# Kernel optimization log

Hardware: AMD Instinct MI355X
Metric: run time of the kernel (lower is better)

## Reference

```python
import jax, jax.numpy as jnp
import numpy as np

B, T, D = 64, 512, 256   # batch, time, input feat
H = 256                  # LSTM hidden (features)


def setup_inputs() -> dict:
    key = jax.random.key(0)
    ks = jax.random.split(key, 16)
    s = lambda k, shp, fan: jax.random.normal(k, shp, jnp.float32) / np.sqrt(fan)
    return {
        "x":  jax.random.normal(ks[0], (B, T, D), jnp.float32),
        # LSTM params: fused gates order (i, f, g, o)
        "Wi": s(ks[1], (D, 4 * H), D),
        "Wh": s(ks[2], (H, 4 * H), H),
        "b":  jnp.zeros((4 * H,), jnp.float32),
        # single-head attention (head_dim = H)
        "Wq": s(ks[3], (H, H), H), "bq": jnp.zeros((H,), jnp.float32),
        "Wk": s(ks[4], (H, H), H), "bk": jnp.zeros((H,), jnp.float32),
        "Wv": s(ks[5], (H, H), H), "bv": jnp.zeros((H,), jnp.float32),
        "Wo": s(ks[6], (H, H), H), "bo": jnp.zeros((H,), jnp.float32),
        # MLP head
        "W1": s(ks[7], (H, 32), H), "b1": jnp.zeros((32,), jnp.float32),
        "W2": s(ks[8], (32, 3), 32), "b2": jnp.zeros((3,), jnp.float32),
    }


def _lstm_scan(x, Wi, Wh, b):
    # Precompute input-to-hidden projection for all timesteps (batched GEMM)
    xg = jnp.einsum('btd,dg->btg', x, Wi) + b          # [B,T,4H]
    c0 = jnp.zeros((x.shape[0], Wh.shape[0]), x.dtype)
    h0 = jnp.zeros_like(c0)

    def step(carry, xg_t):
        c, h = carry
        g = xg_t + h @ Wh                               # [B,4H]
        i, f, gg, o = jnp.split(g, 4, axis=-1)          # flax gate order i,f,g,o
        c = jax.nn.sigmoid(f) * c + jax.nn.sigmoid(i) * jnp.tanh(gg)
        h = jax.nn.sigmoid(o) * jnp.tanh(c)
        return (c, h), h

    (_, _), hs = jax.lax.scan(step, (c0, h0), jnp.swapaxes(xg, 0, 1))
    return jnp.swapaxes(hs, 0, 1)                       # [B,T,H]


def reference(x, Wi, Wh, b, Wq, bq, Wk, bk, Wv, bv, Wo, bo, W1, b1, W2, b2):
    h = _lstm_scan(x, Wi, Wh, b)                        # [B,T,H]
    # single-head dot-product attention (self-attention)
    q = h @ Wq + bq
    k = h @ Wk + bk
    v = h @ Wv + bv
    scale = 1.0 / np.sqrt(q.shape[-1]).astype(np.float32)
    scores = jnp.einsum('bqd,bkd->bqk', q * scale, k)   # [B,T,T]
    attn = jax.nn.softmax(scores, axis=-1)
    o = jnp.einsum('bqk,bkd->bqd', attn, v)
    o = o @ Wo + bo                                     # output projection
    # head on first timestep
    z = jax.nn.relu(o[:, 0, :] @ W1 + b1)
    return z @ W2 + b2                                  # [B,3]
```

## Files before the change

### kernel.cpp

```cpp
#include <hip/hip_runtime.h>
#include <hip/hip_bf16.h>


typedef __attribute__((ext_vector_type(8))) short short8;
typedef __attribute__((ext_vector_type(4))) float float4v;

__device__ __forceinline__ unsigned short f2bf(float f) {
  unsigned u = __builtin_bit_cast(unsigned, f);
  return (unsigned short)((u + 0x7fffu + ((u >> 16) & 1u)) >> 16);
}
__device__ __forceinline__ float bf2f(unsigned short h) {
  return __builtin_bit_cast(float, ((unsigned)h) << 16);
}
__device__ __forceinline__ float bcl(unsigned u) {
  return __builtin_bit_cast(float, u << 16);
}
__device__ __forceinline__ float bch(unsigned u) {
  return __builtin_bit_cast(float, u & 0xffff0000u);
}
__device__ __forceinline__ float sigm(float x) {
  return __builtin_amdgcn_rcpf(1.f + __expf(-x));
}
__device__ __forceinline__ float tanh_f(float x) {
  return 1.f - 2.f * __builtin_amdgcn_rcpf(1.f + __expf(2.f * x));
}

__global__ void prep_all(const float* __restrict__ x,
                         const float* __restrict__ Wi,
                         const float* __restrict__ Wh,
                         unsigned short* __restrict__ xbf,
                         unsigned short* __restrict__ WiT,
                         unsigned short* __restrict__ WhP) {
  const int bid = blockIdx.x, tid = threadIdx.x;
  if (bid < 8192) {
    size_t i = ((size_t)bid * 256 + tid) * 4;
    float4 v = *(const float4*)&x[i];
    unsigned long long pk = (unsigned long long)f2bf(v.x)
                          | ((unsigned long long)f2bf(v.y) << 16)
                          | ((unsigned long long)f2bf(v.z) << 32)
                          | ((unsigned long long)f2bf(v.w) << 48);
    *(unsigned long long*)&xbf[i] = pk;
  } else if (bid < 8448) {
    size_t i = ((size_t)(bid - 8192) * 256 + tid) * 4;
    float4 v = *(const float4*)&Wi[i];
    int k = (int)(i >> 10), n = (int)(i & 1023);
    WiT[(size_t)(n + 0) * 256 + k] = f2bf(v.x);
    WiT[(size_t)(n + 1) * 256 + k] = f2bf(v.y);
    WiT[(size_t)(n + 2) * 256 + k] = f2bf(v.z);
    WiT[(size_t)(n + 3) * 256 + k] = f2bf(v.w);
  } else {
    size_t i0 = ((size_t)(bid - 8448) * 256 + tid) * 4;
    int row = (int)(i0 >> 8);
    int colnat = (row & 3) * 256 + (row >> 7) * 32 + ((row >> 4) & 7) * 4 +
                 ((row >> 2) & 3);
    unsigned long long pk = 0;
#pragma unroll
    for (int j = 0; j < 4; ++j) {
      int k = (int)((i0 + j) & 255);
      pk |= (unsigned long long)f2bf(Wh[(size_t)k * 1024 + colnat]) << (16 * j);
    }
    *(unsigned long long*)&WhP[i0] = pk;
  }
}

#define XKP 40
__global__ __launch_bounds__(256) void xg_gemm(const unsigned short* __restrict__ xbf,
                                               const unsigned short* __restrict__ WiT,
                                               const float* __restrict__ bias,
                                               unsigned short* __restrict__ xg) {
  __shared__ unsigned short As[128 * XKP];
  __shared__ unsigned short Bs[128 * XKP];
  const int tid = threadIdx.x;
  const int n0 = blockIdx.x * 128, m0 = blockIdx.y * 128;
  const int wave = tid >> 6, lane = tid & 63, quad = lane >> 4, l16 = lane & 15;
  const int wm = wave >> 1, wn = wave & 1;

  float4v acc[4][4];
#pragma unroll
  for (int i = 0; i < 4; ++i)
#pragma unroll
    for (int j = 0; j < 4; ++j) acc[i][j] = (float4v){0.f, 0.f, 0.f, 0.f};

  const int rr = tid >> 2, c8 = (tid & 3) * 8;
  for (int k0 = 0; k0 < 256; k0 += 32) {
#pragma unroll
    for (int pp = 0; pp < 2; ++pp) {
      int r = pp * 64 + rr;
      *(uint4*)&As[r * XKP + c8] = *(const uint4*)&xbf[(size_t)(m0 + r) * 256 + k0 + c8];
      *(uint4*)&Bs[r * XKP + c8] = *(const uint4*)&WiT[(size_t)(n0 + r) * 256 + k0 + c8];
    }
    __syncthreads();
#pragma unroll
    for (int mt = 0; mt < 4; ++mt) {
      short8 af = *(const short8*)&As[(wm * 64 + mt * 16 + l16) * XKP + quad * 8];
#pragma unroll
      for (int nt = 0; nt < 4; ++nt) {
        short8 bf = *(const short8*)&Bs[(wn * 64 + nt * 16 + l16) * XKP + quad * 8];
        acc[mt][nt] = __builtin_amdgcn_mfma_f32_16x16x32_bf16(af, bf, acc[mt][nt], 0, 0, 0);
      }
    }
    __syncthreads();
  }
#pragma unroll
  for (int nt = 0; nt < 4; ++nt) {
    int col = n0 + wn * 64 + nt * 16 + l16;
    int gate = col >> 8, u = col & 255;
    float bv = bias[col];
#pragma unroll
    for (int mt = 0; mt < 4; ++mt) {
#pragma unroll
      for (int r = 0; r < 4; ++r) {
        int row = m0 + wm * 64 + mt * 16 + quad * 4 + r;
        int b = row >> 9, t = row & 511;
        xg[(((size_t)b * 512 + t) * 256 + u) * 4 + gate] = f2bf(acc[mt][nt][r] + bv);
      }
    }
  }
}

#define SWZ(rowv, off) ((off) ^ (((rowv) & 7) << 4))
__global__ __launch_bounds__(512, 2) void lstm_scan(
    const unsigned short* __restrict__ WhP,
    const unsigned short* __restrict__ xg,
    unsigned short* __restrict__ hout) {
  __shared__ unsigned short WhL[16 * 16 * 256];
  __shared__ unsigned short hA[256];
  const int tid = threadIdx.x;
  const int b = blockIdx.x;
  const int wave = tid >> 6, lane = tid & 63, quad = lane >> 4, l16 = lane & 15;

  short8 frA[6][8];
  {
    const unsigned short* src = WhP + ((size_t)(wave * 128) + l16) * 256 + quad * 8;
#pragma unroll
    for (int rt = 0; rt < 6; ++rt)
#pragma unroll
      for (int kt = 0; kt < 8; ++kt)
        frA[rt][kt] = *(const short8*)&src[(size_t)rt * 4096 + kt * 32];
  }
  for (int it = 0; it < 16; ++it) {
    int idx = it * 64 + lane;
    int r32 = idx >> 5, ch = idx & 31;
    int tile = wave * 2 + (r32 >> 4), rw = r32 & 15;
    uint4 v = *(const uint4*)&WhP[((size_t)wave * 128 + 96 + r32) * 256 + ch * 8];
    *(uint4*)((char*)WhL + tile * 8192 + rw * 512 + SWZ(rw, ch * 16)) = v;
  }
  for (int i = tid; i < 256; i += 512) hA[i] = 0;
  __syncthreads();

  const bool act = (l16 < 8);
  const int u = wave * 32 + l16 * 4 + quad;
  const unsigned short* xgp = xg + ((size_t)b * 512 * 256 + u) * 4;
  unsigned short* houtp = hout + (size_t)b * 512 * 256 + u;
  float c = 0.f;

  const char* ldsA = (const char*)WhL + (wave * 2) * 8192 + l16 * 512;
  const char* ldsB = ldsA + 8192;

  for (int t = 0; t < 512; ++t) {
    unsigned long long xv = 0;
    if (act) xv = *(const unsigned long long*)&xgp[(size_t)t * 1024];

    float4v acc[8];
#pragma unroll
    for (int rt = 0; rt < 8; ++rt) acc[rt] = (float4v){0.f, 0.f, 0.f, 0.f};

#pragma unroll
    for (int kt = 0; kt < 8; ++kt) {
      short8 hb = *(const short8*)((const char*)hA + kt * 64 + quad * 16);
#pragma unroll
      for (int rt = 0; rt < 6; ++rt)
        acc[rt] = __builtin_amdgcn_mfma_f32_16x16x32_bf16(frA[rt][kt], hb, acc[rt], 0, 0, 0);
      short8 a6 = *(const short8*)(ldsA + SWZ(l16, kt * 64 + quad * 16));
      acc[6] = __builtin_amdgcn_mfma_f32_16x16x32_bf16(a6, hb, acc[6], 0, 0, 0);
      short8 a7 = *(const short8*)(ldsB + SWZ(l16, kt * 64 + quad * 16));
      acc[7] = __builtin_amdgcn_mfma_f32_16x16x32_bf16(a7, hb, acc[7], 0, 0, 0);
    }
    __syncthreads();

    if (act) {
      float4v g4 = acc[0];
#pragma unroll
      for (int rt = 1; rt < 8; ++rt)
        if (l16 == rt) g4 = acc[rt];
      float gi = g4[0] + bf2f((unsigned short)(xv));
      float gf = g4[1] + bf2f((unsigned short)(xv >> 16));
      float gG = g4[2] + bf2f((unsigned short)(xv >> 32));
      float go = g4[3] + bf2f((unsigned short)(xv >> 48));
      float cc = sigm(gf) * c + sigm(gi) * tanh_f(gG);
      c = cc;
      unsigned short hb16 = f2bf(sigm(go) * tanh_f(cc));
      hA[u] = hb16;
      houtp[(size_t)t * 256] = hb16;
    }
    __syncthreads();
  }
}

__global__ __launch_bounds__(256) void attn_head(
    const unsigned short* __restrict__ hout,
    const float* __restrict__ Wq, const float* __restrict__ bq,
    const float* __restrict__ Wk, const float* __restrict__ bk,
    const float* __restrict__ Wv, const float* __restrict__ bv,
    const float* __restrict__ Wo, const float* __restrict__ bo,
    const float* __restrict__ W1, const float* __restrict__ b1,
    const float* __restrict__ W2, const float* __restrict__ b2,
    float* __restrict__ out) {
  __shared__ float h0S[256], q0S[256], red[256], usS[256], sS[512], hb4[4][256];
  __shared__ float oS[256], o1S[256], zS[32], cbS;
  const int b = blockIdx.x, tid = threadIdx.x, wave = tid >> 6, lane = tid & 63;
  const size_t hb_base = (size_t)b * 512 * 256;

  h0S[tid] = bf2f(hout[hb_base + tid]);
  __syncthreads();
  float a = 0.f;
  for (int k = 0; k < 256; ++k) a += h0S[k] * Wq[(size_t)k * 256 + tid];
  q0S[tid] = a + bq[tid];
  __syncthreads();
  red[tid] = q0S[tid] * bk[tid];
  __syncthreads();
  for (int s = 128; s > 0; s >>= 1) {
    if (tid < s) red[tid] += red[tid + s];
    __syncthreads();
  }
  if (tid == 0) cbS = 0.0625f * red[0];
  float acq = 0.f;
  const float* wr = &Wk[(size_t)tid * 256];
  for (int e = 0; e < 256; e += 4) {
    float4 w = *(const float4*)&wr[e];
    acq += w.x * q0S[e] + w.y * q0S[e + 1] + w.z * q0S[e + 2] + w.w * q0S[e + 3];
  }
  usS[tid] = 0.0625f * acq;
  __syncthreads();

  const float u0 = usS[lane * 4 + 0], u1 = usS[lane * 4 + 1];
  const float u2 = usS[lane * 4 + 2], u3 = usS[lane * 4 + 3];
  const float cbv = cbS;
  for (int i = 0; i < 128; ++i) {
    int t = i * 4 + wave;
    unsigned long long hv = *(const unsigned long long*)&hout[hb_base + (size_t)t * 256 + lane * 4];
    unsigned lo = (unsigned)hv, hi = (unsigned)(hv >> 32);
    float p = u0 * bcl(lo) + u1 * bch(lo) + u2 * bcl(hi) + u3 * bch(hi);
    for (int m = 1; m < 64; m <<= 1) p += __shfl_xor(p, m, 64);
    if (lane == 0) sS[t] = p + cbv;
  }
  __syncthreads();
  red[tid] = fmaxf(sS[tid], sS[tid + 256]);
  __syncthreads();
  for (int s = 128; s > 0; s >>= 1) {
    if (tid < s) red[tid] = fmaxf(red[tid], red[tid + s]);
    __syncthreads();
  }
  float mx = red[0];
  __syncthreads();
  float e0 = __expf(sS[tid] - mx), e1 = __expf(sS[tid + 256] - mx);
  sS[tid] = e0; sS[tid + 256] = e1;
  red[tid] = e0 + e1;
  __syncthreads();
  for (int s = 128; s > 0; s >>= 1) {
    if (tid < s) red[tid] += red[tid + s];
    __syncthreads();
  }
  float inv = 1.f / red[0];
  float a0 = 0.f, a1 = 0.f, a2 = 0.f, a3 = 0.f;
  const int d0 = lane * 4;
  for (int i = 0; i < 128; ++i) {
    int t = wave * 128 + i;
    float w = sS[t];
    unsigned long long hv = *(const unsigned long long*)&hout[hb_base + (size_t)t * 256 + d0];
    unsigned lo = (unsigned)hv, hi = (unsigned)(hv >> 32);
    a0 += w * bcl(lo); a1 += w * bch(lo); a2 += w * bcl(hi); a3 += w * bch(hi);
  }
  hb4[wave][d0] = a0; hb4[wave][d0 + 1] = a1; hb4[wave][d0 + 2] = a2; hb4[wave][d0 + 3] = a3;
  __syncthreads();
  h0S[tid] = (hb4[0][tid] + hb4[1][tid] + hb4[2][tid] + hb4[3][tid]) * inv;
  __syncthreads();

  a = 0.f;
  for (int k = 0; k < 256; ++k) a += h0S[k] * Wv[(size_t)k * 256 + tid];
  oS[tid] = a + bv[tid];
  __syncthreads();
  a = 0.f;
  for (int k = 0; k < 256; ++k) a += oS[k] * Wo[(size_t)k * 256 + tid];
  o1S[tid] = a + bo[tid];
  __syncthreads();
  if (tid < 32) {
    a = 0.f;
    for (int k = 0; k < 256; ++k) a += o1S[k] * W1[k * 32 + tid];
    zS[tid] = fmaxf(a + b1[tid], 0.f);
  }
  __syncthreads();
  if (tid < 3) {
    a = 0.f;
    for (int j = 0; j < 32; ++j) a += zS[j] * W2[j * 3 + tid];
    out[b * 3 + tid] = a + b2[tid];
  }
}

extern "C" void kernel_launch(void* const* d_in, const int* in_sizes, int n_in,
                              void* d_out, int out_size, void* d_ws, size_t ws_size,
                              hipStream_t stream) {
  const float* x  = (const float*)d_in[0];
  const float* Wi = (const float*)d_in[1];
  const float* Wh = (const float*)d_in[2];
  const float* bG = (const float*)d_in[3];
  const float* Wq = (const float*)d_in[4];
  const float* bq = (const float*)d_in[5];
  const float* Wk = (const float*)d_in[6];
  const float* bk = (const float*)d_in[7];
  const float* Wv = (const float*)d_in[8];
  const float* bv = (const float*)d_in[9];
  const float* Wo = (const float*)d_in[10];
  const float* bo = (const float*)d_in[11];
  const float* W1 = (const float*)d_in[12];
  const float* b1 = (const float*)d_in[13];
  const float* W2 = (const float*)d_in[14];
  const float* b2 = (const float*)d_in[15];
  float* out = (float*)d_out;
  char* ws = (char*)d_ws;

  unsigned short* xg   = (unsigned short*)(ws);
  unsigned short* hout = (unsigned short*)(ws + 67108864);
  unsigned short* xbf  = (unsigned short*)(ws + 83886080);
  unsigned short* WiT  = (unsigned short*)(ws + 100663296);
  unsigned short* WhP  = (unsigned short*)(ws + 101187584);

  prep_all<<<dim3(8704), dim3(256), 0, stream>>>(x, Wi, Wh, xbf, WiT, WhP);
  xg_gemm<<<dim3(8, 256), dim3(256), 0, stream>>>(xbf, WiT, bG, xg);
  lstm_scan<<<dim3(64), dim3(512), 0, stream>>>(WhP, xg, hout);
  attn_head<<<dim3(64), dim3(256), 0, stream>>>(hout, Wq, bq, Wk, bk, Wv, bv,
                                                Wo, bo, W1, b1, W2, b2, out);
}
```

Measured before the change: 1.352 ms.

## Split LSTM scan over 16 waves with double-buffered h and batched output stores

The recurrent scan now runs with 1024 threads per batch row, so each wave owns 64 gate rows instead of 128. This halves the per-wave MFMA chain per timestep, and the Wh permutation is remapped to match. The hidden state is double-buffered, which drops one of the two block barriers per step. Per-step global stores of h are replaced by a shared staging buffer that is flushed as coalesced 16-row chunks. In exchange, the wider block adds barrier cost across 16 waves and uses more LDS per block.

```diff
diff --git a/kernel.cpp b/kernel.cpp
--- a/kernel.cpp
+++ b/kernel.cpp
@@ -51,7 +51,7 @@
   } else {
     size_t i0 = ((size_t)(bid - 8448) * 256 + tid) * 4;
     int row = (int)(i0 >> 8);
-    int colnat = (row & 3) * 256 + (row >> 7) * 32 + ((row >> 4) & 7) * 4 +
+    int colnat = (row & 3) * 256 + (row >> 6) * 16 + ((row >> 4) & 3) * 4 +
                  ((row >> 2) & 3);
     unsigned long long pk = 0;
 #pragma unroll
@@ -118,82 +118,90 @@
   }
 }
 
-#define SWZ(rowv, off) ((off) ^ (((rowv) & 7) << 4))
-__global__ __launch_bounds__(512, 2) void lstm_scan(
+__global__ __launch_bounds__(1024) void lstm_scan(
     const unsigned short* __restrict__ WhP,
     const unsigned short* __restrict__ xg,
     unsigned short* __restrict__ hout) {
-  __shared__ unsigned short WhL[16 * 16 * 256];
-  __shared__ unsigned short hA[256];
+  __shared__ unsigned short WhL[16 * 4096];
+  __shared__ unsigned short hA[2][256];
+  __shared__ unsigned short hoB[2][16][256];
   const int tid = threadIdx.x;
   const int b = blockIdx.x;
   const int wave = tid >> 6, lane = tid & 63, quad = lane >> 4, l16 = lane & 15;
 
-  short8 frA[6][8];
+  short8 frA[3][8];
   {
-    const unsigned short* src = WhP + ((size_t)(wave * 128) + l16) * 256 + quad * 8;
-#pragma unroll
-    for (int rt = 0; rt < 6; ++rt)
+    const unsigned short* src = WhP + ((size_t)wave * 64 + l16) * 256 + quad * 8;
+#pragma unroll
+    for (int rt = 0; rt < 3; ++rt)
 #pragma unroll
       for (int kt = 0; kt < 8; ++kt)
-        frA[rt][kt] = *(const short8*)&src[(size_t)rt * 4096 + kt * 32];
-  }
-  for (int it = 0; it < 16; ++it) {
-    int idx = it * 64 + lane;
-    int r32 = idx >> 5, ch = idx & 31;
-    int tile = wave * 2 + (r32 >> 4), rw = r32 & 15;
-    uint4 v = *(const uint4*)&WhP[((size_t)wave * 128 + 96 + r32) * 256 + ch * 8];
-    *(uint4*)((char*)WhL + tile * 8192 + rw * 512 + SWZ(rw, ch * 16)) = v;
-  }
-  for (int i = tid; i < 256; i += 512) hA[i] = 0;
-  __syncthreads();
-
-  const bool act = (l16 < 8);
-  const int u = wave * 32 + l16 * 4 + quad;
+        frA[rt][kt] = *(const short8*)&src[rt * 4096 + kt * 32];
+  }
+#pragma unroll
+  for (int i = 0; i < 8; ++i) {
+    int idx = i * 64 + lane;
+    int rw = idx >> 5, ch = idx & 31;
+    uint4 v = *(const uint4*)&WhP[((size_t)wave * 64 + 48 + rw) * 256 + ch * 8];
+    *(uint4*)((char*)WhL + wave * 8192 + rw * 512 + ((ch * 16) ^ ((rw & 7) << 4))) = v;
+  }
+  if (tid < 512) ((unsigned short*)hA)[tid] = 0;
+
+  const bool act = (l16 < 4);
+  const int u = wave * 16 + l16 * 4 + quad;
   const unsigned short* xgp = xg + ((size_t)b * 512 * 256 + u) * 4;
-  unsigned short* houtp = hout + (size_t)b * 512 * 256 + u;
+  unsigned short* houtb = hout + (size_t)b * 512 * 256;
+  const char* tileA = (const char*)WhL + wave * 8192 + l16 * 512;
   float c = 0.f;
 
-  const char* ldsA = (const char*)WhL + (wave * 2) * 8192 + l16 * 512;
-  const char* ldsB = ldsA + 8192;
+  __syncthreads();
 
   for (int t = 0; t < 512; ++t) {
     unsigned long long xv = 0;
-    if (act) xv = *(const unsigned long long*)&xgp[(size_t)t * 1024];
-
-    float4v acc[8];
-#pragma unroll
-    for (int rt = 0; rt < 8; ++rt) acc[rt] = (float4v){0.f, 0.f, 0.f, 0.f};
-
+    if (act) xv = *(const unsigned long long*)(xgp + (size_t)t * 1024);
+
+    if ((t & 15) == 0 && t) {
+      int hf = ((t >> 4) & 1) ^ 1;
+      int row = tid >> 6, u0 = (lane) * 4;
+      unsigned long long hv = *(const unsigned long long*)&hoB[hf][row][u0];
+      *(unsigned long long*)&houtb[(size_t)(t - 16 + row) * 256 + u0] = hv;
+    }
+
+    const unsigned short* hbuf = hA[t & 1];
+    float4v acc[4];
+#pragma unroll
+    for (int rt = 0; rt < 4; ++rt) acc[rt] = (float4v){0.f, 0.f, 0.f, 0.f};
 #pragma unroll
     for (int kt = 0; kt < 8; ++kt) {
-      short8 hb = *(const short8*)((const char*)hA + kt * 64 + quad * 16);
-#pragma unroll
-      for (int rt = 0; rt < 6; ++rt)
-        acc[rt] = __builtin_amdgcn_mfma_f32_16x16x32_bf16(frA[rt][kt], hb, acc[rt], 0, 0, 0);
-      short8 a6 = *(const short8*)(ldsA + SWZ(l16, kt * 64 + quad * 16));
-      acc[6] = __builtin_amdgcn_mfma_f32_16x16x32_bf16(a6, hb, acc[6], 0, 0, 0);
-      short8 a7 = *(const short8*)(ldsB + SWZ(l16, kt * 64 + quad * 16));
-      acc[7] = __builtin_amdgcn_mfma_f32_16x16x32_bf16(a7, hb, acc[7], 0, 0, 0);
-    }
-    __syncthreads();
+      short8 hb = *(const short8*)((const char*)hbuf + kt * 64 + quad * 16);
+      acc[0] = __builtin_amdgcn_mfma_f32_16x16x32_bf16(frA[0][kt], hb, acc[0], 0, 0, 0);
+      acc[1] = __builtin_amdgcn_mfma_f32_16x16x32_bf16(frA[1][kt], hb, acc[1], 0, 0, 0);
+      acc[2] = __builtin_amdgcn_mfma_f32_16x16x32_bf16(frA[2][kt], hb, acc[2], 0, 0, 0);
+      short8 a3 = *(const short8*)(tileA + ((kt * 64 + quad * 16) ^ ((l16 & 7) << 4)));
+      acc[3] = __builtin_amdgcn_mfma_f32_16x16x32_bf16(a3, hb, acc[3], 0, 0, 0);
+    }
 
     if (act) {
       float4v g4 = acc[0];
-#pragma unroll
-      for (int rt = 1; rt < 8; ++rt)
-        if (l16 == rt) g4 = acc[rt];
+      if (l16 == 1) g4 = acc[1];
+      if (l16 == 2) g4 = acc[2];
+      if (l16 == 3) g4 = acc[3];
       float gi = g4[0] + bf2f((unsigned short)(xv));
       float gf = g4[1] + bf2f((unsigned short)(xv >> 16));
       float gG = g4[2] + bf2f((unsigned short)(xv >> 32));
       float go = g4[3] + bf2f((unsigned short)(xv >> 48));
       float cc = sigm(gf) * c + sigm(gi) * tanh_f(gG);
       c = cc;
-      unsigned short hb16 = f2bf(sigm(go) * tanh_f(cc));
-      hA[u] = hb16;
-      houtp[(size_t)t * 256] = hb16;
-    }
-    __syncthreads();
+      unsigned short h16 = f2bf(sigm(go) * tanh_f(cc));
+      hA[(t + 1) & 1][u] = h16;
+      hoB[(t >> 4) & 1][t & 15][u] = h16;
+    }
+    __syncthreads();
+  }
+  {
+    int row = tid >> 6, u0 = (lane) * 4;
+    unsigned long long hv = *(const unsigned long long*)&hoB[1][row][u0];
+    *(unsigned long long*)&houtb[(size_t)(496 + row) * 256 + u0] = hv;
   }
 }
 
@@ -327,7 +335,7 @@
 
   prep_all<<<dim3(8704), dim3(256), 0, stream>>>(x, Wi, Wh, xbf, WiT, WhP);
   xg_gemm<<<dim3(8, 256), dim3(256), 0, stream>>>(xbf, WiT, bG, xg);
-  lstm_scan<<<dim3(64), dim3(512), 0, stream>>>(WhP, xg, hout);
+  lstm_scan<<<dim3(64), dim3(1024), 0, stream>>>(WhP, xg, hout);
   attn_head<<<dim3(64), dim3(256), 0, stream>>>(hout, Wq, bq, Wk, bk, Wv, bv,
                                                 Wo, bo, W1, b1, W2, b2, out);
 }
```

New measurement: 2.295 ms. +69.7%, slower.

## Restructure LSTM scan to 4 waves with double-buffered hidden state

Applied to the files above, without the earlier changes.

The recurrent scan kernel moves from 8 waves to 4 waves per batch row. Each wave now owns 64 hidden units, keeps 12 weight tiles in registers, and streams 4 tiles from swizzled LDS. The hidden-state buffer is double-buffered, so each timestep needs one barrier instead of two, and all lanes now do gate math with no idle half. The cost is much higher register pressure: 96 short8 fragments plus 8 more LDS-loaded ones per gate quad. Serial MFMA work per wave also doubles, which may lengthen the per-step critical path.

```diff
diff --git a/kernel.cpp b/kernel.cpp
--- a/kernel.cpp
+++ b/kernel.cpp
@@ -51,7 +51,7 @@
   } else {
     size_t i0 = ((size_t)(bid - 8448) * 256 + tid) * 4;
     int row = (int)(i0 >> 8);
-    int colnat = (row & 3) * 256 + (row >> 7) * 32 + ((row >> 4) & 7) * 4 +
+    int colnat = (row & 3) * 256 + (row >> 8) * 64 + ((row >> 4) & 15) * 4 +
                  ((row >> 2) & 3);
     unsigned long long pk = 0;
 #pragma unroll
@@ -118,81 +118,88 @@
   }
 }
 
-#define SWZ(rowv, off) ((off) ^ (((rowv) & 7) << 4))
-__global__ __launch_bounds__(512, 2) void lstm_scan(
+__global__ __launch_bounds__(256, 1) void lstm_scan(
     const unsigned short* __restrict__ WhP,
     const unsigned short* __restrict__ xg,
     unsigned short* __restrict__ hout) {
-  __shared__ unsigned short WhL[16 * 16 * 256];
-  __shared__ unsigned short hA[256];
+  __shared__ unsigned short WhL[16 * 4096];
+  __shared__ unsigned short hA[2][256];
   const int tid = threadIdx.x;
   const int b = blockIdx.x;
   const int wave = tid >> 6, lane = tid & 63, quad = lane >> 4, l16 = lane & 15;
 
-  short8 frA[6][8];
-  {
-    const unsigned short* src = WhP + ((size_t)(wave * 128) + l16) * 256 + quad * 8;
-#pragma unroll
-    for (int rt = 0; rt < 6; ++rt)
+  short8 frA[12][8];
+#pragma unroll
+  for (int gq = 0; gq < 4; ++gq)
+#pragma unroll
+    for (int j = 0; j < 3; ++j) {
+      const int rtid = gq * 4 + j;
+      const unsigned short* src =
+          WhP + ((size_t)wave * 256 + rtid * 16 + l16) * 256 + quad * 8;
 #pragma unroll
       for (int kt = 0; kt < 8; ++kt)
-        frA[rt][kt] = *(const short8*)&src[(size_t)rt * 4096 + kt * 32];
-  }
-  for (int it = 0; it < 16; ++it) {
-    int idx = it * 64 + lane;
-    int r32 = idx >> 5, ch = idx & 31;
-    int tile = wave * 2 + (r32 >> 4), rw = r32 & 15;
-    uint4 v = *(const uint4*)&WhP[((size_t)wave * 128 + 96 + r32) * 256 + ch * 8];
-    *(uint4*)((char*)WhL + tile * 8192 + rw * 512 + SWZ(rw, ch * 16)) = v;
-  }
-  for (int i = tid; i < 256; i += 512) hA[i] = 0;
-  __syncthreads();
-
-  const bool act = (l16 < 8);
-  const int u = wave * 32 + l16 * 4 + quad;
+        frA[gq * 3 + j][kt] = *(const short8*)&src[kt * 32];
+    }
+#pragma unroll
+  for (int i = 0; i < 32; ++i) {
+    int gq = i >> 3;
+    int chunk = (i & 7) * 64 + lane;
+    int rw = chunk >> 5, ch = chunk & 31;
+    uint4 v = *(const uint4*)&WhP[((size_t)wave * 256 + (gq * 4 + 3) * 16 + rw) * 256 + ch * 8];
+    *(uint4*)((char*)WhL + (wave * 4 + gq) * 8192 + rw * 512 +
+              ((ch * 16) ^ ((rw & 7) << 4))) = v;
+  }
+  ((unsigned short*)hA)[tid] = 0;
+  ((unsigned short*)hA)[tid + 256] = 0;
+  __syncthreads();
+
+  const int u = wave * 64 + l16 * 4 + quad;
   const unsigned short* xgp = xg + ((size_t)b * 512 * 256 + u) * 4;
   unsigned short* houtp = hout + (size_t)b * 512 * 256 + u;
+  const char* ldsT = (const char*)WhL + wave * 4 * 8192 + l16 * 512;
   float c = 0.f;
 
-  const char* ldsA = (const char*)WhL + (wave * 2) * 8192 + l16 * 512;
-  const char* ldsB = ldsA + 8192;
-
   for (int t = 0; t < 512; ++t) {
-    unsigned long long xv = 0;
-    if (act) xv = *(const unsigned long long*)&xgp[(size_t)t * 1024];
-
-    float4v acc[8];
-#pragma unroll
-    for (int rt = 0; rt < 8; ++rt) acc[rt] = (float4v){0.f, 0.f, 0.f, 0.f};
-
-#pragma unroll
-    for (int kt = 0; kt < 8; ++kt) {
-      short8 hb = *(const short8*)((const char*)hA + kt * 64 + quad * 16);
-#pragma unroll
-      for (int rt = 0; rt < 6; ++rt)
-        acc[rt] = __builtin_amdgcn_mfma_f32_16x16x32_bf16(frA[rt][kt], hb, acc[rt], 0, 0, 0);
-      short8 a6 = *(const short8*)(ldsA + SWZ(l16, kt * 64 + quad * 16));
-      acc[6] = __builtin_amdgcn_mfma_f32_16x16x32_bf16(a6, hb, acc[6], 0, 0, 0);
-      short8 a7 = *(const short8*)(ldsB + SWZ(l16, kt * 64 + quad * 16));
-      acc[7] = __builtin_amdgcn_mfma_f32_16x16x32_bf16(a7, hb, acc[7], 0, 0, 0);
-    }
-    __syncthreads();
-
-    if (act) {
-      float4v g4 = acc[0];
-#pragma unroll
-      for (int rt = 1; rt < 8; ++rt)
-        if (l16 == rt) g4 = acc[rt];
-      float gi = g4[0] + bf2f((unsigned short)(xv));
-      float gf = g4[1] + bf2f((unsigned short)(xv >> 16));
-      float gG = g4[2] + bf2f((unsigned short)(xv >> 32));
-      float go = g4[3] + bf2f((unsigned short)(xv >> 48));
-      float cc = sigm(gf) * c + sigm(gi) * tanh_f(gG);
-      c = cc;
-      unsigned short hb16 = f2bf(sigm(go) * tanh_f(cc));
-      hA[u] = hb16;
-      houtp[(size_t)t * 256] = hb16;
-    }
+    unsigned long long xv = *(const unsigned long long*)(xgp + (size_t)t * 1024);
+
+    const char* hbuf = (const char*)hA[t & 1];
+    short8 hb8[8];
+#pragma unroll
+    for (int kt = 0; kt < 8; ++kt)
+      hb8[kt] = *(const short8*)(hbuf + kt * 64 + quad * 16);
+
+    float4v g4 = (float4v){0.f, 0.f, 0.f, 0.f};
+#pragma unroll
+    for (int gq = 0; gq < 4; ++gq) {
+      short8 al[8];
+#pragma unroll
+      for (int kt = 0; kt < 8; ++kt)
+        al[kt] = *(const short8*)(ldsT + gq * 8192 +
+                                  ((kt * 64 + quad * 16) ^ ((l16 & 7) << 4)));
+      float4v a0 = (float4v){0.f, 0.f, 0.f, 0.f};
+      float4v a1 = a0, a2 = a0, a3 = a0;
+#pragma unroll
+      for (int kt = 0; kt < 8; ++kt) {
+        a0 = __builtin_amdgcn_mfma_f32_16x16x32_bf16(frA[gq * 3 + 0][kt], hb8[kt], a0, 0, 0, 0);
+        a1 = __builtin_amdgcn_mfma_f32_16x16x32_bf16(frA[gq * 3 + 1][kt], hb8[kt], a1, 0, 0, 0);
+        a2 = __builtin_amdgcn_mfma_f32_16x16x32_bf16(frA[gq * 3 + 2][kt], hb8[kt], a2, 0, 0, 0);
+        a3 = __builtin_amdgcn_mfma_f32_16x16x32_bf16(al[kt], hb8[kt], a3, 0, 0, 0);
+      }
+      if (l16 == gq * 4 + 0) g4 = a0;
+      if (l16 == gq * 4 + 1) g4 = a1;
+      if (l16 == gq * 4 + 2) g4 = a2;
+      if (l16 == gq * 4 + 3) g4 = a3;
+    }
+
+    float gi = g4[0] + bf2f((unsigned short)(xv));
+    float gf = g4[1] + bf2f((unsigned short)(xv >> 16));
+    float gG = g4[2] + bf2f((unsigned short)(xv >> 32));
+    float go = g4[3] + bf2f((unsigned short)(xv >> 48));
+    float cc = sigm(gf) * c + sigm(gi) * tanh_f(gG);
+    c = cc;
+    unsigned short h16 = f2bf(sigm(go) * tanh_f(cc));
+    hA[(t + 1) & 1][u] = h16;
+    houtp[(size_t)t * 256] = h16;
     __syncthreads();
   }
 }
@@ -327,7 +334,7 @@
 
   prep_all<<<dim3(8704), dim3(256), 0, stream>>>(x, Wi, Wh, xbf, WiT, WhP);
   xg_gemm<<<dim3(8, 256), dim3(256), 0, stream>>>(xbf, WiT, bG, xg);
-  lstm_scan<<<dim3(64), dim3(512), 0, stream>>>(WhP, xg, hout);
+  lstm_scan<<<dim3(64), dim3(256), 0, stream>>>(WhP, xg, hout);
   attn_head<<<dim3(64), dim3(256), 0, stream>>>(hout, Wq, bq, Wk, bk, Wv, bv,
                                                 Wo, bo, W1, b1, W2, b2, out);
 }
```

Result: slower. 1.475 ms (+9.1%).
